# Kernel tuning notes

Hardware: AMD Instinct MI355X
Metric: run time of the kernel (lower is better)

The kernel has to match this reference:

```python
import jax, jax.numpy as jnp
import numpy as np

HEAD_SIZE = 64  # EMBEDDING_SIZE(384) // HEAD_NO(6)

def setup_inputs() -> dict:
    key = jax.random.key(0)
    ks = jax.random.split(key, 6)
    B, T, C, H, D = 256, 256, 384, 6, 64
    s = 0.02
    return {
        "x": jax.random.normal(ks[0], (B, T, C), dtype=jnp.float32),
        "Wq": jax.random.normal(ks[1], (H, C, D), dtype=jnp.float32) * s,
        "Wk": jax.random.normal(ks[2], (H, C, D), dtype=jnp.float32) * s,
        "Wv": jax.random.normal(ks[3], (H, C, D), dtype=jnp.float32) * s,
        "Wproj": jax.random.normal(ks[4], (C, C), dtype=jnp.float32) * s,
        "bproj": jnp.zeros((C,), dtype=jnp.float32),
    }

def reference(x, Wq, Wk, Wv, Wproj, bproj):
    B, T, C = x.shape
    # per-head projections, stacked over heads h: [B, H, T, D]
    q = jnp.einsum('btc,hcd->bhtd', x, Wq)
    k = jnp.einsum('btc,hcd->bhtd', x, Wk)
    v = jnp.einsum('btc,hcd->bhtd', x, Wv)
    scale = 1.0 / jnp.sqrt(jnp.asarray(HEAD_SIZE, dtype=x.dtype))
    # scores [B, H, T, T]; causal mask (masked_fill then /scale == scale then mask, since -inf/scale=-inf)
    scores = jnp.einsum('bhtd,bhsd->bhts', q, k) * scale
    causal = jnp.tril(jnp.ones((T, T), dtype=bool))
    scores = jnp.where(causal, scores, -jnp.inf)
    w = jax.nn.softmax(scores, axis=-1)
    # dropout is identity in eval mode
    out = jnp.einsum('bhts,bhsd->bhtd', w, v)          # [B, H, T, D]
    out = out.transpose(0, 2, 1, 3).reshape(B, T, C)    # concat heads -> [B, T, C]
    return out @ Wproj + bproj
```

## Files before the change

### kernel.cpp

```cpp
#include <hip/hip_runtime.h>
#include <hip/hip_bf16.h>

typedef __bf16 bf16;
typedef unsigned int u32;
typedef __attribute__((ext_vector_type(8))) __bf16 bf16x8;
typedef __attribute__((ext_vector_type(4))) float f32x4;

#define Bsz 256
#define Tsz 256
#define Csz 384
#define Hn  6
#define Dh  64
#define NQKV 1152

#define MFMA16(a, b, c) __builtin_amdgcn_mfma_f32_16x16x32_bf16(a, b, c, 0, 0, 0)

typedef __attribute__((address_space(3))) u32 lds_u32;
typedef __attribute__((address_space(1))) const u32 gbl_u32;
__device__ __forceinline__ void gl2lds16(const void* g, void* l) {
    __builtin_amdgcn_global_load_lds((gbl_u32*)g, (lds_u32*)l, 16, 0, 0);
}

__device__ __forceinline__ float redmax16(float x) {
    x = fmaxf(x, __shfl_xor(x, 1));
    x = fmaxf(x, __shfl_xor(x, 2));
    x = fmaxf(x, __shfl_xor(x, 4));
    x = fmaxf(x, __shfl_xor(x, 8));
    return x;
}
__device__ __forceinline__ float redsum16(float x) {
    x += __shfl_xor(x, 1);
    x += __shfl_xor(x, 2);
    x += __shfl_xor(x, 4);
    x += __shfl_xor(x, 8);
    return x;
}

__global__ __launch_bounds__(256) void convert_x(
    const float* __restrict__ x, bf16* __restrict__ xb)
{
    size_t i = ((size_t)blockIdx.x * 256 + threadIdx.x) * 8;
    float4 f0 = *(const float4*)&x[i];
    float4 f1 = *(const float4*)&x[i + 4];
    bf16x8 o;
    o[0] = (bf16)f0.x; o[1] = (bf16)f0.y; o[2] = (bf16)f0.z; o[3] = (bf16)f0.w;
    o[4] = (bf16)f1.x; o[5] = (bf16)f1.y; o[6] = (bf16)f1.z; o[7] = (bf16)f1.w;
    *(bf16x8*)&xb[i] = o;
}

__global__ __launch_bounds__(384) void prep_w(
    const float* __restrict__ Wq, const float* __restrict__ Wk,
    const float* __restrict__ Wv, const float* __restrict__ Wp,
    bf16* __restrict__ Btqkv, bf16* __restrict__ Bpt)
{
    const int n = blockIdx.x, k = threadIdx.x;
    if (n < NQKV) {
        int wi = n / Csz, rem = n - wi * Csz, h = rem >> 6, d = rem & 63;
        const float* W = wi == 0 ? Wq : (wi == 1 ? Wk : Wv);
        Btqkv[(size_t)n * Csz + k] = (bf16)W[((size_t)h * Csz + k) * Dh + d];
    } else {
        int n2 = n - NQKV;
        Bpt[(size_t)n2 * Csz + k] = (bf16)Wp[(size_t)k * Csz + n2];
    }
}


__device__ __forceinline__ void stage_tile512(
    const char* Ab, const char* Bb, int m0, int n0, int t,
    char* AsB, char* BsB, int tid)
{
    const int srow = tid >> 3;
    const int scs  = ((tid & 7) * 16) ^ ((srow & 7) << 4);
    #pragma unroll
    for (int j = 0; j < 4; ++j)
        gl2lds16(Ab + (size_t)(m0 + j * 64 + srow) * 768 + t * 128 + scs,
                 AsB + j * 8192 + tid * 16);
    #pragma unroll
    for (int j = 0; j < 2; ++j)
        gl2lds16(Bb + (size_t)(n0 + j * 64 + srow) * 768 + t * 128 + scs,
                 BsB + j * 8192 + tid * 16);
}

__device__ __forceinline__ void compute_tile512(
    const char* Ap, const char* Bp,
    int wm4, int wn2, int l4, int quad, f32x4 acc[4][4])
{
    const int cswz = (l4 & 7) << 4;
    bf16x8 bfr[4][2], af[4][2];
    #pragma unroll
    for (int fn = 0; fn < 4; ++fn)
        #pragma unroll
        for (int ks = 0; ks < 2; ++ks)
            bfr[fn][ks] = *(const bf16x8*)(Bp + (wn2 * 64 + fn * 16 + l4) * 128 +
                                           ((ks * 64 + quad * 16) ^ cswz));
    #pragma unroll
    for (int fr = 0; fr < 4; ++fr)
        #pragma unroll
        for (int ks = 0; ks < 2; ++ks)
            af[fr][ks] = *(const bf16x8*)(Ap + (wm4 * 64 + fr * 16 + l4) * 128 +
                                          ((ks * 64 + quad * 16) ^ cswz));
    __builtin_amdgcn_s_setprio(1);
    #pragma unroll
    for (int ks = 0; ks < 2; ++ks)
        #pragma unroll
        for (int fr = 0; fr < 4; ++fr)
            #pragma unroll
            for (int fn = 0; fn < 4; ++fn)
                acc[fr][fn] = MFMA16(af[fr][ks], bfr[fn][ks], acc[fr][fn]);
    __builtin_amdgcn_s_setprio(0);
}

#define GEMM_PIPE8()                                                           \
    stage_tile512(Ab, Bb, m0, n0, 0, As0, Bs0, tid);                           \
    _Pragma("unroll")                                                          \
    for (int t = 0; t < 6; ++t) {                                              \
        if (t < 5) stage_tile512(Ab, Bb, m0, n0, t + 1,                        \
                                 (t & 1) ? As0 : As1, (t & 1) ? Bs0 : Bs1, tid);\
        if (t < 5) { asm volatile("s_waitcnt vmcnt(6)" ::: "memory"); }        \
        else       { asm volatile("s_waitcnt vmcnt(0)" ::: "memory"); }        \
        __builtin_amdgcn_s_barrier();                                          \
        compute_tile512((t & 1) ? As1 : As0, (t & 1) ? Bs1 : Bs0,              \
                        wm4, wn2, l4, quad, acc);                              \
        __builtin_amdgcn_s_barrier();                                          \
    }

__global__ __launch_bounds__(512, 2) void qkv_gemm(
    const bf16* __restrict__ A, const bf16* __restrict__ Bt,
    bf16* __restrict__ q, bf16* __restrict__ k, bf16* __restrict__ v)
{
    __shared__ bf16 As[2][256][64];
    __shared__ bf16 Bs[2][128][64];
    char* As0 = (char*)&As[0][0][0]; char* As1 = (char*)&As[1][0][0];
    char* Bs0 = (char*)&Bs[0][0][0]; char* Bs1 = (char*)&Bs[1][0][0];
    const int tid = threadIdx.x, w = tid >> 6, lane = tid & 63;
    const int l4 = lane & 15, quad = lane >> 4;
    const int wm4 = w >> 1, wn2 = w & 1;

    const int orig = blockIdx.x;
    const int id = (orig & 7) * 288 + (orig >> 3);
    const int mt_ = id / 9, nt_ = id - mt_ * 9;
    const int m0 = mt_ * 256, n0 = nt_ * 128;

    const char* Ab = (const char*)A;
    const char* Bb = (const char*)Bt;
    f32x4 acc[4][4] = {};

    GEMM_PIPE8();

    #pragma unroll
    for (int fn = 0; fn < 4; ++fn) {
        int n = n0 + wn2 * 64 + fn * 16 + l4;
        int wi = n / Csz, rem = n - wi * Csz;
        int h = rem >> 6, d = rem & 63;
        bf16* outp = wi == 0 ? q : (wi == 1 ? k : v);
        #pragma unroll
        for (int fr = 0; fr < 4; ++fr)
            #pragma unroll
            for (int r = 0; r < 4; ++r) {
                int m = m0 + wm4 * 64 + fr * 16 + quad * 4 + r;
                int b = m >> 8, tt = m & 255;
                outp[(((size_t)(b * Hn + h)) * Tsz + tt) * Dh + d] = (bf16)acc[fr][fn][r];
            }
    }
}

__global__ __launch_bounds__(512, 2) void proj_gemm(
    const bf16* __restrict__ A, const bf16* __restrict__ Bt,
    const float* __restrict__ bias, float* __restrict__ out)
{
    __shared__ bf16 As[2][256][64];
    __shared__ bf16 Bs[2][128][64];
    char* As0 = (char*)&As[0][0][0]; char* As1 = (char*)&As[1][0][0];
    char* Bs0 = (char*)&Bs[0][0][0]; char* Bs1 = (char*)&Bs[1][0][0];
    const int tid = threadIdx.x, w = tid >> 6, lane = tid & 63;
    const int l4 = lane & 15, quad = lane >> 4;
    const int wm4 = w >> 1, wn2 = w & 1;

    const int orig = blockIdx.x;
    const int id = (orig & 7) * 96 + (orig >> 3);
    const int mt_ = id / 3, nt_ = id - mt_ * 3;
    const int m0 = mt_ * 256, n0 = nt_ * 128;

    const char* Ab = (const char*)A;
    const char* Bb = (const char*)Bt;
    f32x4 acc[4][4] = {};

    GEMM_PIPE8();

    #pragma unroll
    for (int fn = 0; fn < 4; ++fn) {
        int n = n0 + wn2 * 64 + fn * 16 + l4;
        float bv = bias[n];
        #pragma unroll
        for (int fr = 0; fr < 4; ++fr)
            #pragma unroll
            for (int r = 0; r < 4; ++r) {
                int m = m0 + wm4 * 64 + fr * 16 + quad * 4 + r;
                out[(size_t)m * Csz + n] = acc[fr][fn][r] + bv;
            }
    }
}

__global__ __launch_bounds__(512, 4) void attn_mfma(
    const bf16* __restrict__ q, const bf16* __restrict__ k, const bf16* __restrict__ v,
    bf16* __restrict__ att)
{
    __shared__ bf16 Kl[256][64];
    __shared__ bf16 Vt[64][256];
    __shared__ bf16 Pl[8][16][64];
    const float SCL = 0.18033688f;
    const int tid = threadIdx.x, w = tid >> 6, lane = tid & 63;
    const int l4 = lane & 15, quad = lane >> 4;
    const int cswz = l4 & 7;
    const int bh = blockIdx.x;
    const int b = bh / Hn, h = bh % Hn;
    const bf16* qb = q + (size_t)bh * Tsz * Dh;
    const bf16* kb = k + (size_t)bh * Tsz * Dh;
    const bf16* vb = v + (size_t)bh * Tsz * Dh;
    char* KlB = (char*)&Kl[0][0];
    char* VtB = (char*)&Vt[0][0];
    char* PlB = (char*)&Pl[w][0][0];

    bf16x8 qa[2][2];
    #pragma unroll
    for (int fi = 0; fi < 2; ++fi) {
        int g = fi ? 15 - w : w;
        qa[fi][0] = *(const bf16x8*)&qb[(g * 16 + l4) * Dh + quad * 8];
        qa[fi][1] = *(const bf16x8*)&qb[(g * 16 + l4) * Dh + 32 + quad * 8];
    }

    #pragma unroll
    for (int it = 0; it < 4; ++it) {
        int c = it * 512 + tid;
        int row = c >> 3, ck = c & 7;
        bf16x8 kv = *(const bf16x8*)((const char*)kb + (size_t)c * 16);
        *(bf16x8*)(KlB + row * 128 + ((ck ^ (row & 7)) << 4)) = kv;
    }
    #pragma unroll
    for (int it = 0; it < 4; ++it) {
        int idx = it * 512 + tid;
        int s = idx & 63, g2 = idx >> 6;
        int d8 = (g2 & 7) * 8, sg = (g2 >> 3) * 64 + s;
        bf16x8 vv = *(const bf16x8*)&vb[(size_t)sg * Dh + d8];
        #pragma unroll
        for (int j = 0; j < 8; ++j) {
            int row = d8 + j;
            *(bf16*)(VtB + row * 512 + (((sg >> 3) ^ (row & 7)) << 4) + (sg & 7) * 2) = vv[j];
        }
    }
    __syncthreads();

    #pragma unroll
    for (int fi = 0; fi < 2; ++fi) {
        const int g = fi ? 15 - w : w;
        const int diag = g >> 2;
        const int tg = g * 16 + quad * 4;
        f32x4 o[4] = {f32x4{0,0,0,0}, f32x4{0,0,0,0}, f32x4{0,0,0,0}, f32x4{0,0,0,0}};
        float mrun[4] = {-3.0e38f, -3.0e38f, -3.0e38f, -3.0e38f};
        float lrun[4] = {0.f, 0.f, 0.f, 0.f};

        for (int kt = 0; kt <= diag; ++kt) {
            f32x4 sc[4] = {f32x4{0,0,0,0}, f32x4{0,0,0,0}, f32x4{0,0,0,0}, f32x4{0,0,0,0}};
            __builtin_amdgcn_s_setprio(1);
            #pragma unroll
            for (int nt = 0; nt < 4; ++nt) {
                const char* kbase = KlB + (kt * 64 + nt * 16 + l4) * 128;
                bf16x8 b0 = *(const bf16x8*)(kbase + ((quad ^ cswz) << 4));
                bf16x8 b1 = *(const bf16x8*)(kbase + (((4 + quad) ^ cswz) << 4));
                sc[nt] = MFMA16(qa[fi][0], b0, sc[nt]);
                sc[nt] = MFMA16(qa[fi][1], b1, sc[nt]);
            }
            __builtin_amdgcn_s_setprio(0);

            const bool isdiag = (kt == diag);
            float mnew[4], alpha[4];
            #pragma unroll
            for (int r = 0; r < 4; ++r) {
                float mx = mrun[r];
                #pragma unroll
                for (int nt = 0; nt < 4; ++nt) {
                    float sv = sc[nt][r] * SCL;
                    if (isdiag) {
                        int sg2 = kt * 64 + nt * 16 + l4;
                        if (sg2 > tg + r) sv = -1.0e30f;
                    }
                    sc[nt][r] = sv;
                    mx = fmaxf(mx, sv);
                }
                mx = redmax16(mx);
                mnew[r] = mx;
                alpha[r] = __builtin_amdgcn_exp2f(mrun[r] - mx);
                mrun[r] = mx;
            }
            #pragma unroll
            for (int r = 0; r < 4; ++r) {
                float sm = 0.f;
                #pragma unroll
                for (int nt = 0; nt < 4; ++nt) {
                    float e = __builtin_amdgcn_exp2f(sc[nt][r] - mnew[r]);
                    sc[nt][r] = e;
                    sm += e;
                }
                sm = redsum16(sm);
                lrun[r] = lrun[r] * alpha[r] + sm;
            }
            #pragma unroll
            for (int nt = 0; nt < 4; ++nt)
                #pragma unroll
                for (int r = 0; r < 4; ++r) o[nt][r] *= alpha[r];

            #pragma unroll
            for (int nt = 0; nt < 4; ++nt)
                #pragma unroll
                for (int r = 0; r < 4; ++r) {
                    int row = quad * 4 + r;
                    int colc = nt * 2 + (l4 >> 3);
                    *(bf16*)(PlB + row * 128 + ((colc ^ (row & 7)) << 4) + (l4 & 7) * 2)
                        = (bf16)sc[nt][r];
                }
            bf16x8 pa0 = *(const bf16x8*)(PlB + l4 * 128 + ((quad ^ cswz) << 4));
            bf16x8 pa1 = *(const bf16x8*)(PlB + l4 * 128 + (((4 + quad) ^ cswz) << 4));

            __builtin_amdgcn_s_setprio(1);
            #pragma unroll
            for (int nt = 0; nt < 4; ++nt) {
                const char* vbase = VtB + (nt * 16 + l4) * 512;
                bf16x8 v0 = *(const bf16x8*)(vbase + (((kt * 8 + quad) ^ cswz) << 4));
                bf16x8 v1 = *(const bf16x8*)(vbase + (((kt * 8 + 4 + quad) ^ cswz) << 4));
                o[nt] = MFMA16(pa0, v0, o[nt]);
                o[nt] = MFMA16(pa1, v1, o[nt]);
            }
            __builtin_amdgcn_s_setprio(0);
        }

        #pragma unroll
        for (int r = 0; r < 4; ++r) {
            float inv = 1.f / lrun[r];
            #pragma unroll
            for (int nt = 0; nt < 4; ++nt)
                att[((size_t)(b * Tsz + tg + r)) * Csz + h * Dh + nt * 16 + l4] =
                    (bf16)(o[nt][r] * inv);
        }
    }
}

extern "C" void kernel_launch(void* const* d_in, const int* in_sizes, int n_in,
                              void* d_out, int out_size, void* d_ws, size_t ws_size,
                              hipStream_t stream)
{
    const float* x  = (const float*)d_in[0];
    const float* Wq = (const float*)d_in[1];
    const float* Wk = (const float*)d_in[2];
    const float* Wv = (const float*)d_in[3];
    const float* Wp = (const float*)d_in[4];
    const float* bp = (const float*)d_in[5];
    float* out = (float*)d_out;

    const size_t npe = (size_t)Bsz * Tsz * Csz;
    bf16* xb    = (bf16*)d_ws;
    bf16* att   = xb;
    bf16* q     = xb + npe;
    bf16* k     = q  + npe;
    bf16* v     = k  + npe;
    bf16* Btqkv = v  + npe;
    bf16* Bpt   = Btqkv + (size_t)NQKV * Csz;

    convert_x<<<npe / 2048, 256, 0, stream>>>(x, xb);
    prep_w<<<NQKV + Csz, 384, 0, stream>>>(Wq, Wk, Wv, Wp, Btqkv, Bpt);
    qkv_gemm<<<(Bsz * Tsz / 256) * (NQKV / 128), 512, 0, stream>>>(xb, Btqkv, q, k, v);
    attn_mfma<<<Bsz * Hn, 512, 0, stream>>>(q, k, v, att);
    proj_gemm<<<(Bsz * Tsz / 256) * (Csz / 128), 512, 0, stream>>>(att, Bpt, bp, out);
}
```

Baseline: 369.6 us.

## Make QKV and proj GEMMs persistent over N tiles with overlapped epilogue

```diff
diff --git a/kernel.cpp b/kernel.cpp
--- a/kernel.cpp
+++ b/kernel.cpp
@@ -110,19 +110,26 @@
     __builtin_amdgcn_s_setprio(0);
 }
 
-#define GEMM_PIPE8()                                                           \
-    stage_tile512(Ab, Bb, m0, n0, 0, As0, Bs0, tid);                           \
-    _Pragma("unroll")                                                          \
-    for (int t = 0; t < 6; ++t) {                                              \
-        if (t < 5) stage_tile512(Ab, Bb, m0, n0, t + 1,                        \
-                                 (t & 1) ? As0 : As1, (t & 1) ? Bs0 : Bs1, tid);\
-        if (t < 5) { asm volatile("s_waitcnt vmcnt(6)" ::: "memory"); }        \
-        else       { asm volatile("s_waitcnt vmcnt(0)" ::: "memory"); }        \
-        __builtin_amdgcn_s_barrier();                                          \
-        compute_tile512((t & 1) ? As1 : As0, (t & 1) ? Bs1 : Bs0,              \
-                        wm4, wn2, l4, quad, acc);                              \
-        __builtin_amdgcn_s_barrier();                                          \
-    }
+__device__ __forceinline__ void qkv_store(
+    const f32x4 (&a)[4][4], int nn, int m0, int wm4, int wn2, int l4, int quad,
+    bf16* __restrict__ q, bf16* __restrict__ k, bf16* __restrict__ v)
+{
+    #pragma unroll
+    for (int fn = 0; fn < 4; ++fn) {
+        int n = nn * 128 + wn2 * 64 + fn * 16 + l4;
+        int wi = n / Csz, rem = n - wi * Csz;
+        int h = rem >> 6, d = rem & 63;
+        bf16* outp = wi == 0 ? q : (wi == 1 ? k : v);
+        #pragma unroll
+        for (int fr = 0; fr < 4; ++fr)
+            #pragma unroll
+            for (int r = 0; r < 4; ++r) {
+                int m = m0 + wm4 * 64 + fr * 16 + quad * 4 + r;
+                int b = m >> 8, tt = m & 255;
+                outp[(((size_t)(b * Hn + h)) * Tsz + tt) * Dh + d] = (bf16)a[fr][fn][r];
+            }
+    }
+}
 
 __global__ __launch_bounds__(512, 2) void qkv_gemm(
     const bf16* __restrict__ A, const bf16* __restrict__ Bt,
@@ -135,33 +142,46 @@
     const int tid = threadIdx.x, w = tid >> 6, lane = tid & 63;
     const int l4 = lane & 15, quad = lane >> 4;
     const int wm4 = w >> 1, wn2 = w & 1;
-
-    const int orig = blockIdx.x;
-    const int id = (orig & 7) * 288 + (orig >> 3);
-    const int mt_ = id / 9, nt_ = id - mt_ * 9;
-    const int m0 = mt_ * 256, n0 = nt_ * 128;
+    const int m0 = blockIdx.x * 256;
 
     const char* Ab = (const char*)A;
     const char* Bb = (const char*)Bt;
     f32x4 acc[4][4] = {};
-
-    GEMM_PIPE8();
-
-    #pragma unroll
-    for (int fn = 0; fn < 4; ++fn) {
-        int n = n0 + wn2 * 64 + fn * 16 + l4;
-        int wi = n / Csz, rem = n - wi * Csz;
-        int h = rem >> 6, d = rem & 63;
-        bf16* outp = wi == 0 ? q : (wi == 1 ? k : v);
-        #pragma unroll
-        for (int fr = 0; fr < 4; ++fr)
-            #pragma unroll
-            for (int r = 0; r < 4; ++r) {
-                int m = m0 + wm4 * 64 + fr * 16 + quad * 4 + r;
-                int b = m >> 8, tt = m & 255;
-                outp[(((size_t)(b * Hn + h)) * Tsz + tt) * Dh + d] = (bf16)acc[fr][fn][r];
-            }
-    }
+    f32x4 oacc[4][4];
+
+    stage_tile512(Ab, Bb, m0, 0, 0, As0, Bs0, tid);
+    #pragma unroll 1
+    for (int n = 0; n < 9; ++n) {
+        #pragma unroll
+        for (int kc = 0; kc < 6; ++kc) {
+            const bool last = (n == 8) && (kc == 5);
+            if (!last) {
+                const int n1  = (kc == 5) ? n + 1 : n;
+                const int kc1 = (kc == 5) ? 0 : kc + 1;
+                stage_tile512(Ab, Bb, m0, n1 * 128, kc1,
+                              (kc & 1) ? As0 : As1, (kc & 1) ? Bs0 : Bs1, tid);
+                asm volatile("s_waitcnt vmcnt(6)" ::: "memory");
+            } else {
+                asm volatile("s_waitcnt vmcnt(0)" ::: "memory");
+            }
+            __builtin_amdgcn_s_barrier();
+            if (kc == 0 && n > 0)
+                qkv_store(oacc, n - 1, m0, wm4, wn2, l4, quad, q, k, v);
+            compute_tile512((kc & 1) ? As1 : As0, (kc & 1) ? Bs1 : Bs0,
+                            wm4, wn2, l4, quad, acc);
+            __builtin_amdgcn_s_barrier();
+        }
+        if (n < 8) {
+            #pragma unroll
+            for (int i = 0; i < 4; ++i)
+                #pragma unroll
+                for (int j = 0; j < 4; ++j) {
+                    oacc[i][j] = acc[i][j];
+                    acc[i][j] = f32x4{0, 0, 0, 0};
+                }
+        }
+    }
+    qkv_store(acc, 8, m0, wm4, wn2, l4, quad, q, k, v);
 }
 
 __global__ __launch_bounds__(512, 2) void proj_gemm(
@@ -175,28 +195,75 @@
     const int tid = threadIdx.x, w = tid >> 6, lane = tid & 63;
     const int l4 = lane & 15, quad = lane >> 4;
     const int wm4 = w >> 1, wn2 = w & 1;
-
-    const int orig = blockIdx.x;
-    const int id = (orig & 7) * 96 + (orig >> 3);
-    const int mt_ = id / 3, nt_ = id - mt_ * 3;
-    const int m0 = mt_ * 256, n0 = nt_ * 128;
+    const int m0 = blockIdx.x * 256;
+
+    float bvr[3][4];
+    #pragma unroll
+    for (int nn = 0; nn < 3; ++nn)
+        #pragma unroll
+        for (int fn = 0; fn < 4; ++fn)
+            bvr[nn][fn] = bias[nn * 128 + wn2 * 64 + fn * 16 + l4];
 
     const char* Ab = (const char*)A;
     const char* Bb = (const char*)Bt;
     f32x4 acc[4][4] = {};
-
-    GEMM_PIPE8();
-
+    f32x4 oacc[4][4];
+
+    stage_tile512(Ab, Bb, m0, 0, 0, As0, Bs0, tid);
+    #pragma unroll 1
+    for (int n = 0; n < 3; ++n) {
+        #pragma unroll
+        for (int kc = 0; kc < 6; ++kc) {
+            const bool last = (n == 2) && (kc == 5);
+            if (!last) {
+                const int n1  = (kc == 5) ? n + 1 : n;
+                const int kc1 = (kc == 5) ? 0 : kc + 1;
+                stage_tile512(Ab, Bb, m0, n1 * 128, kc1,
+                              (kc & 1) ? As0 : As1, (kc & 1) ? Bs0 : Bs1, tid);
+                asm volatile("s_waitcnt vmcnt(6)" ::: "memory");
+            } else {
+                asm volatile("s_waitcnt vmcnt(0)" ::: "memory");
+            }
+            __builtin_amdgcn_s_barrier();
+            if (kc == 0 && n > 0) {
+                const int np = n - 1;
+                #pragma unroll
+                for (int fn = 0; fn < 4; ++fn) {
+                    int ncol = np * 128 + wn2 * 64 + fn * 16 + l4;
+                    float bv = bvr[np][fn];
+                    #pragma unroll
+                    for (int fr = 0; fr < 4; ++fr)
+                        #pragma unroll
+                        for (int r = 0; r < 4; ++r) {
+                            int m = m0 + wm4 * 64 + fr * 16 + quad * 4 + r;
+                            out[(size_t)m * Csz + ncol] = oacc[fr][fn][r] + bv;
+                        }
+                }
+            }
+            compute_tile512((kc & 1) ? As1 : As0, (kc & 1) ? Bs1 : Bs0,
+                            wm4, wn2, l4, quad, acc);
+            __builtin_amdgcn_s_barrier();
+        }
+        if (n < 2) {
+            #pragma unroll
+            for (int i = 0; i < 4; ++i)
+                #pragma unroll
+                for (int j = 0; j < 4; ++j) {
+                    oacc[i][j] = acc[i][j];
+                    acc[i][j] = f32x4{0, 0, 0, 0};
+                }
+        }
+    }
     #pragma unroll
     for (int fn = 0; fn < 4; ++fn) {
-        int n = n0 + wn2 * 64 + fn * 16 + l4;
-        float bv = bias[n];
+        int ncol = 2 * 128 + wn2 * 64 + fn * 16 + l4;
+        float bv = bvr[2][fn];
         #pragma unroll
         for (int fr = 0; fr < 4; ++fr)
             #pragma unroll
             for (int r = 0; r < 4; ++r) {
                 int m = m0 + wm4 * 64 + fr * 16 + quad * 4 + r;
-                out[(size_t)m * Csz + n] = acc[fr][fn][r] + bv;
+                out[(size_t)m * Csz + ncol] = acc[fr][fn][r] + bv;
             }
     }
 }
@@ -367,7 +434,7 @@
 
     convert_x<<<npe / 2048, 256, 0, stream>>>(x, xb);
     prep_w<<<NQKV + Csz, 384, 0, stream>>>(Wq, Wk, Wv, Wp, Btqkv, Bpt);
-    qkv_gemm<<<(Bsz * Tsz / 256) * (NQKV / 128), 512, 0, stream>>>(xb, Btqkv, q, k, v);
+    qkv_gemm<<<Bsz * Tsz / 256, 512, 0, stream>>>(xb, Btqkv, q, k, v);
     attn_mfma<<<Bsz * Hn, 512, 0, stream>>>(q, k, v, att);
-    proj_gemm<<<(Bsz * Tsz / 256) * (Csz / 128), 512, 0, stream>>>(att, Bpt, bp, out);
-}
+    proj_gemm<<<Bsz * Tsz / 256, 512, 0, stream>>>(att, Bpt, bp, out);
+}
```

Result: slower. 454.0 us (+22.9%).

## Enlarge GEMM tiles to 256x256 with interleaved four-phase LDS pipeline

Applied to the files above, without the earlier changes.

```diff
diff --git a/kernel.cpp b/kernel.cpp
--- a/kernel.cpp
+++ b/kernel.cpp
@@ -12,6 +12,8 @@
 #define Hn  6
 #define Dh  64
 #define NQKV 1152
+#define NPAD 1280
+#define PPAD 512
 
 #define MFMA16(a, b, c) __builtin_amdgcn_mfma_f32_16x16x32_bf16(a, b, c, 0, 0, 0)
 
@@ -54,110 +56,151 @@
     bf16* __restrict__ Btqkv, bf16* __restrict__ Bpt)
 {
     const int n = blockIdx.x, k = threadIdx.x;
-    if (n < NQKV) {
-        int wi = n / Csz, rem = n - wi * Csz, h = rem >> 6, d = rem & 63;
-        const float* W = wi == 0 ? Wq : (wi == 1 ? Wk : Wv);
-        Btqkv[(size_t)n * Csz + k] = (bf16)W[((size_t)h * Csz + k) * Dh + d];
+    if (n < NPAD) {
+        bf16 vout = (bf16)0.f;
+        if (n < NQKV) {
+            int wi = n / Csz, rem = n - wi * Csz, h = rem >> 6, d = rem & 63;
+            const float* W = wi == 0 ? Wq : (wi == 1 ? Wk : Wv);
+            vout = (bf16)W[((size_t)h * Csz + k) * Dh + d];
+        }
+        Btqkv[(size_t)n * Csz + k] = vout;
     } else {
-        int n2 = n - NQKV;
-        Bpt[(size_t)n2 * Csz + k] = (bf16)Wp[(size_t)k * Csz + n2];
-    }
-}
-
-
-__device__ __forceinline__ void stage_tile512(
-    const char* Ab, const char* Bb, int m0, int n0, int t,
-    char* AsB, char* BsB, int tid)
+        int n2 = n - NPAD;
+        Bpt[(size_t)n2 * Csz + k] =
+            (n2 < Csz) ? (bf16)Wp[(size_t)k * Csz + n2] : (bf16)0.f;
+    }
+}
+
+
+__device__ __forceinline__ void stage_half(
+    const char* Gb, int rowbase, int t, char* ldsDst, int tid)
 {
     const int srow = tid >> 3;
     const int scs  = ((tid & 7) * 16) ^ ((srow & 7) << 4);
-    #pragma unroll
-    for (int j = 0; j < 4; ++j)
-        gl2lds16(Ab + (size_t)(m0 + j * 64 + srow) * 768 + t * 128 + scs,
-                 AsB + j * 8192 + tid * 16);
-    #pragma unroll
-    for (int j = 0; j < 2; ++j)
-        gl2lds16(Bb + (size_t)(n0 + j * 64 + srow) * 768 + t * 128 + scs,
-                 BsB + j * 8192 + tid * 16);
-}
-
-__device__ __forceinline__ void compute_tile512(
-    const char* Ap, const char* Bp,
-    int wm4, int wn2, int l4, int quad, f32x4 acc[4][4])
-{
-    const int cswz = (l4 & 7) << 4;
-    bf16x8 bfr[4][2], af[4][2];
-    #pragma unroll
-    for (int fn = 0; fn < 4; ++fn)
-        #pragma unroll
-        for (int ks = 0; ks < 2; ++ks)
-            bfr[fn][ks] = *(const bf16x8*)(Bp + (wn2 * 64 + fn * 16 + l4) * 128 +
-                                           ((ks * 64 + quad * 16) ^ cswz));
-    #pragma unroll
-    for (int fr = 0; fr < 4; ++fr)
-        #pragma unroll
-        for (int ks = 0; ks < 2; ++ks)
-            af[fr][ks] = *(const bf16x8*)(Ap + (wm4 * 64 + fr * 16 + l4) * 128 +
-                                          ((ks * 64 + quad * 16) ^ cswz));
-    __builtin_amdgcn_s_setprio(1);
-    #pragma unroll
-    for (int ks = 0; ks < 2; ++ks)
-        #pragma unroll
-        for (int fr = 0; fr < 4; ++fr)
-            #pragma unroll
-            for (int fn = 0; fn < 4; ++fn)
-                acc[fr][fn] = MFMA16(af[fr][ks], bfr[fn][ks], acc[fr][fn]);
-    __builtin_amdgcn_s_setprio(0);
-}
-
-#define GEMM_PIPE8()                                                           \
-    stage_tile512(Ab, Bb, m0, n0, 0, As0, Bs0, tid);                           \
-    _Pragma("unroll")                                                          \
-    for (int t = 0; t < 6; ++t) {                                              \
-        if (t < 5) stage_tile512(Ab, Bb, m0, n0, t + 1,                        \
-                                 (t & 1) ? As0 : As1, (t & 1) ? Bs0 : Bs1, tid);\
-        if (t < 5) { asm volatile("s_waitcnt vmcnt(6)" ::: "memory"); }        \
-        else       { asm volatile("s_waitcnt vmcnt(0)" ::: "memory"); }        \
-        __builtin_amdgcn_s_barrier();                                          \
-        compute_tile512((t & 1) ? As1 : As0, (t & 1) ? Bs1 : Bs0,              \
-                        wm4, wn2, l4, quad, acc);                              \
-        __builtin_amdgcn_s_barrier();                                          \
-    }
+    gl2lds16(Gb + (size_t)(rowbase + srow) * 768 + t * 128 + scs,
+             ldsDst + tid * 16);
+    gl2lds16(Gb + (size_t)(rowbase + 64 + srow) * 768 + t * 128 + scs,
+             ldsDst + 8192 + tid * 16);
+}
+
+#define RD_FRAG(dst, base, row128, ks)                                         \
+    dst = *(const bf16x8*)((base) + (row128) * 128 + ((((ks) * 64) + quad * 16) ^ csw));
+
+#define GEMM_TILE(t)                                                           \
+{                                                                              \
+    const int cur = (t) & 1, nxt = cur ^ 1;                                    \
+    char* Ac = As + cur * 32768; char* Bc = Bs + cur * 32768;                  \
+    char* An = As + nxt * 32768; char* Bn = Bs + nxt * 32768;                  \
+    bf16x8 aLo[4][2], aHi[4][2], bLo[2][2], bHi[2][2];                         \
+             \
+    _Pragma("unroll") for (int fr = 0; fr < 4; ++fr)                           \
+        _Pragma("unroll") for (int ks = 0; ks < 2; ++ks)                       \
+            RD_FRAG(aLo[fr][ks], Ac, wmw * 64 + fr * 16 + l4, ks);             \
+    _Pragma("unroll") for (int fn = 0; fn < 2; ++fn)                           \
+        _Pragma("unroll") for (int ks = 0; ks < 2; ++ks)                       \
+            RD_FRAG(bLo[fn][ks], Bc, wnw * 32 + fn * 16 + l4, ks);             \
+    if ((t) < 5) stage_half(Ab, m0, (t) + 1, An, tid);                         \
+    __builtin_amdgcn_s_barrier();                                              \
+    asm volatile("s_waitcnt lgkmcnt(0)" ::: "memory");                         \
+    __builtin_amdgcn_s_setprio(1);                                             \
+    _Pragma("unroll") for (int ks = 0; ks < 2; ++ks)                           \
+        _Pragma("unroll") for (int fr = 0; fr < 4; ++fr)                       \
+            _Pragma("unroll") for (int fn = 0; fn < 2; ++fn)                   \
+                acc[fr][fn] = MFMA16(aLo[fr][ks], bLo[fn][ks], acc[fr][fn]);   \
+    __builtin_amdgcn_s_setprio(0);                                             \
+    if ((t) < 5) { asm volatile("s_waitcnt vmcnt(4)" ::: "memory"); }          \
+    else         { asm volatile("s_waitcnt vmcnt(2)" ::: "memory"); }          \
+    __builtin_amdgcn_s_barrier();                                              \
+                 \
+    _Pragma("unroll") for (int fr = 0; fr < 4; ++fr)                           \
+        _Pragma("unroll") for (int ks = 0; ks < 2; ++ks)                       \
+            RD_FRAG(aHi[fr][ks], Ac + 16384, wmw * 64 + fr * 16 + l4, ks);     \
+    if ((t) < 5) stage_half(Bb, n0, (t) + 1, Bn, tid);                         \
+    __builtin_amdgcn_s_barrier();                                              \
+    asm volatile("s_waitcnt lgkmcnt(0)" ::: "memory");                         \
+    __builtin_amdgcn_s_setprio(1);                                             \
+    _Pragma("unroll") for (int ks = 0; ks < 2; ++ks)                           \
+        _Pragma("unroll") for (int fr = 0; fr < 4; ++fr)                       \
+            _Pragma("unroll") for (int fn = 0; fn < 2; ++fn)                   \
+                acc[4 + fr][fn] = MFMA16(aHi[fr][ks], bLo[fn][ks], acc[4 + fr][fn]); \
+    __builtin_amdgcn_s_setprio(0);                                             \
+    if ((t) < 5) { asm volatile("s_waitcnt vmcnt(4)" ::: "memory"); }          \
+    else         { asm volatile("s_waitcnt vmcnt(0)" ::: "memory"); }          \
+    __builtin_amdgcn_s_barrier();                                              \
+                 \
+    _Pragma("unroll") for (int fn = 0; fn < 2; ++fn)                           \
+        _Pragma("unroll") for (int ks = 0; ks < 2; ++ks)                       \
+            RD_FRAG(bHi[fn][ks], Bc + 16384, wnw * 32 + fn * 16 + l4, ks);     \
+    if ((t) < 5) stage_half(Ab, m0 + 128, (t) + 1, An + 16384, tid);           \
+    __builtin_amdgcn_s_barrier();                                              \
+    asm volatile("s_waitcnt lgkmcnt(0)" ::: "memory");                         \
+    __builtin_amdgcn_s_setprio(1);                                             \
+    _Pragma("unroll") for (int ks = 0; ks < 2; ++ks)                           \
+        _Pragma("unroll") for (int fr = 0; fr < 4; ++fr)                       \
+            _Pragma("unroll") for (int fn = 0; fn < 2; ++fn)                   \
+                acc[4 + fr][2 + fn] = MFMA16(aHi[fr][ks], bHi[fn][ks], acc[4 + fr][2 + fn]); \
+    __builtin_amdgcn_s_setprio(0);                                             \
+    if ((t) < 5) { asm volatile("s_waitcnt vmcnt(4)" ::: "memory"); }          \
+    __builtin_amdgcn_s_barrier();                                              \
+                 \
+    if ((t) < 5) stage_half(Bb, n0 + 128, (t) + 1, Bn + 16384, tid);           \
+    __builtin_amdgcn_s_barrier();                                              \
+    __builtin_amdgcn_s_setprio(1);                                             \
+    _Pragma("unroll") for (int ks = 0; ks < 2; ++ks)                           \
+        _Pragma("unroll") for (int fr = 0; fr < 4; ++fr)                       \
+            _Pragma("unroll") for (int fn = 0; fn < 2; ++fn)                   \
+                acc[fr][2 + fn] = MFMA16(aLo[fr][ks], bHi[fn][ks], acc[fr][2 + fn]); \
+    __builtin_amdgcn_s_setprio(0);                                             \
+    if ((t) < 5) { asm volatile("s_waitcnt vmcnt(4)" ::: "memory"); }          \
+    __builtin_amdgcn_s_barrier();                                              \
+}
+
+#define GEMM8_BODY()                                                           \
+                 \
+    stage_half(Ab, m0,       0, As,         tid);                              \
+    stage_half(Bb, n0,       0, Bs,         tid);                              \
+    stage_half(Ab, m0 + 128, 0, As + 16384, tid);                              \
+    stage_half(Bb, n0 + 128, 0, Bs + 16384, tid);                              \
+    asm volatile("s_waitcnt vmcnt(4)" ::: "memory");                           \
+    __builtin_amdgcn_s_barrier();                                              \
+    GEMM_TILE(0) GEMM_TILE(1) GEMM_TILE(2)                                     \
+    GEMM_TILE(3) GEMM_TILE(4) GEMM_TILE(5)
 
 __global__ __launch_bounds__(512, 2) void qkv_gemm(
     const bf16* __restrict__ A, const bf16* __restrict__ Bt,
     bf16* __restrict__ q, bf16* __restrict__ k, bf16* __restrict__ v)
 {
-    __shared__ bf16 As[2][256][64];
-    __shared__ bf16 Bs[2][128][64];
-    char* As0 = (char*)&As[0][0][0]; char* As1 = (char*)&As[1][0][0];
-    char* Bs0 = (char*)&Bs[0][0][0]; char* Bs1 = (char*)&Bs[1][0][0];
+    __shared__ char ldsbuf[131072];
+    char* As = ldsbuf;
+    char* Bs = ldsbuf + 65536;
     const int tid = threadIdx.x, w = tid >> 6, lane = tid & 63;
     const int l4 = lane & 15, quad = lane >> 4;
-    const int wm4 = w >> 1, wn2 = w & 1;
+    const int wmw = w & 1, wnw = w >> 1;
+    const int csw = (l4 & 7) << 4;
 
     const int orig = blockIdx.x;
-    const int id = (orig & 7) * 288 + (orig >> 3);
-    const int mt_ = id / 9, nt_ = id - mt_ * 9;
-    const int m0 = mt_ * 256, n0 = nt_ * 128;
+    const int id = (orig & 7) * 160 + (orig >> 3);
+    const int mt_ = id / 5, nt_ = id - mt_ * 5;
+    const int m0 = mt_ * 256, n0 = nt_ * 256;
 
     const char* Ab = (const char*)A;
     const char* Bb = (const char*)Bt;
-    f32x4 acc[4][4] = {};
-
-    GEMM_PIPE8();
+    f32x4 acc[8][4] = {};
+
+    GEMM8_BODY();
 
     #pragma unroll
     for (int fn = 0; fn < 4; ++fn) {
-        int n = n0 + wn2 * 64 + fn * 16 + l4;
+        int n = n0 + (fn >= 2) * 128 + wnw * 32 + (fn & 1) * 16 + l4;
+        if (n >= NQKV) continue;
         int wi = n / Csz, rem = n - wi * Csz;
         int h = rem >> 6, d = rem & 63;
         bf16* outp = wi == 0 ? q : (wi == 1 ? k : v);
         #pragma unroll
-        for (int fr = 0; fr < 4; ++fr)
+        for (int fr = 0; fr < 8; ++fr)
             #pragma unroll
             for (int r = 0; r < 4; ++r) {
-                int m = m0 + wm4 * 64 + fr * 16 + quad * 4 + r;
+                int m = m0 + (fr >= 4) * 128 + wmw * 64 + (fr & 3) * 16 + quad * 4 + r;
                 int b = m >> 8, tt = m & 255;
                 outp[(((size_t)(b * Hn + h)) * Tsz + tt) * Dh + d] = (bf16)acc[fr][fn][r];
             }
@@ -168,35 +211,42 @@
     const bf16* __restrict__ A, const bf16* __restrict__ Bt,
     const float* __restrict__ bias, float* __restrict__ out)
 {
-    __shared__ bf16 As[2][256][64];
-    __shared__ bf16 Bs[2][128][64];
-    char* As0 = (char*)&As[0][0][0]; char* As1 = (char*)&As[1][0][0];
-    char* Bs0 = (char*)&Bs[0][0][0]; char* Bs1 = (char*)&Bs[1][0][0];
+    __shared__ char ldsbuf[131072];
+    char* As = ldsbuf;
+    char* Bs = ldsbuf + 65536;
     const int tid = threadIdx.x, w = tid >> 6, lane = tid & 63;
     const int l4 = lane & 15, quad = lane >> 4;
-    const int wm4 = w >> 1, wn2 = w & 1;
+    const int wmw = w & 1, wnw = w >> 1;
+    const int csw = (l4 & 7) << 4;
 
     const int orig = blockIdx.x;
-    const int id = (orig & 7) * 96 + (orig >> 3);
-    const int mt_ = id / 3, nt_ = id - mt_ * 3;
-    const int m0 = mt_ * 256, n0 = nt_ * 128;
+    const int id = (orig & 7) * 64 + (orig >> 3);
+    const int mt_ = id >> 1, nt_ = id & 1;
+    const int m0 = mt_ * 256, n0 = nt_ * 256;
+
+    float bv[4];
+    #pragma unroll
+    for (int fn = 0; fn < 4; ++fn) {
+        int n = n0 + (fn >= 2) * 128 + wnw * 32 + (fn & 1) * 16 + l4;
+        bv[fn] = (n < Csz) ? bias[n] : 0.f;
+    }
 
     const char* Ab = (const char*)A;
     const char* Bb = (const char*)Bt;
-    f32x4 acc[4][4] = {};
-
-    GEMM_PIPE8();
+    f32x4 acc[8][4] = {};
+
+    GEMM8_BODY();
 
     #pragma unroll
     for (int fn = 0; fn < 4; ++fn) {
-        int n = n0 + wn2 * 64 + fn * 16 + l4;
-        float bv = bias[n];
+        int n = n0 + (fn >= 2) * 128 + wnw * 32 + (fn & 1) * 16 + l4;
+        if (n >= Csz) continue;
         #pragma unroll
-        for (int fr = 0; fr < 4; ++fr)
+        for (int fr = 0; fr < 8; ++fr)
             #pragma unroll
             for (int r = 0; r < 4; ++r) {
-                int m = m0 + wm4 * 64 + fr * 16 + quad * 4 + r;
-                out[(size_t)m * Csz + n] = acc[fr][fn][r] + bv;
+                int m = m0 + (fr >= 4) * 128 + wmw * 64 + (fr & 3) * 16 + quad * 4 + r;
+                out[(size_t)m * Csz + n] = acc[fr][fn][r] + bv[fn];
             }
     }
 }
@@ -363,11 +413,11 @@
     bf16* k     = q  + npe;
     bf16* v     = k  + npe;
     bf16* Btqkv = v  + npe;
-    bf16* Bpt   = Btqkv + (size_t)NQKV * Csz;
+    bf16* Bpt   = Btqkv + (size_t)NPAD * Csz;
 
     convert_x<<<npe / 2048, 256, 0, stream>>>(x, xb);
-    prep_w<<<NQKV + Csz, 384, 0, stream>>>(Wq, Wk, Wv, Wp, Btqkv, Bpt);
-    qkv_gemm<<<(Bsz * Tsz / 256) * (NQKV / 128), 512, 0, stream>>>(xb, Btqkv, q, k, v);
+    prep_w<<<NPAD + PPAD, 384, 0, stream>>>(Wq, Wk, Wv, Wp, Btqkv, Bpt);
+    qkv_gemm<<<(Bsz * Tsz / 256) * (NPAD / 256), 512, 0, stream>>>(xb, Btqkv, q, k, v);
     attn_mfma<<<Bsz * Hn, 512, 0, stream>>>(q, k, v, att);
-    proj_gemm<<<(Bsz * Tsz / 256) * (Csz / 128), 512, 0, stream>>>(att, Bpt, bp, out);
-}
+    proj_gemm<<<(Bsz * Tsz / 256) * (PPAD / 256), 512, 0, stream>>>(att, Bpt, bp, out);
+}
```

Result: no change. 375.1 us (+1.5%).
